# Optimization experiments

Measured on AMD Instinct MI355X. Metric: run time of the kernel, lower is better.

## Reference

```python
import jax, jax.numpy as jnp
import numpy as np

NUM_CELLS = 1_000_000
NUM_NETS = 1_500_000
NUM_PINS = 6_000_000
BOARD = 1000.0   # board_size
GAMMA = 4.0      # LSE smoothing parameter from __init__


def setup_inputs() -> dict:
    key = jax.random.key(0)
    k1, k2, k3, k4 = jax.random.split(key, 4)
    cells_pos = jax.random.uniform(k1, (NUM_CELLS, 2), dtype=jnp.float32) * BOARD
    pin_offsets = jax.random.normal(k2, (NUM_PINS, 2), dtype=jnp.float32) * 0.5
    pin_cell = jax.random.randint(k3, (NUM_PINS,), 0, NUM_CELLS)
    pin_net = jnp.sort(jax.random.randint(k4, (NUM_PINS,), 0, NUM_NETS))
    return {"cells_pos": cells_pos, "pin_offsets": pin_offsets,
            "pin_cell": pin_cell, "pin_net": pin_net}


def _seg_lse(vals, seg, num_segments, gamma):
    # per-segment  gamma * logsumexp(vals / gamma), numerically stable.
    m = jax.ops.segment_max(vals, seg, num_segments=num_segments,
                            indices_are_sorted=True)
    empty = jnp.isneginf(m)                     # segments with no pins
    m_safe = jnp.where(empty, 0.0, m)
    s = jax.ops.segment_sum(jnp.exp((vals - m_safe[seg]) / gamma), seg,
                            num_segments=num_segments, indices_are_sorted=True)
    lse = m_safe + gamma * jnp.log(jnp.maximum(s, 1e-30))
    return jnp.where(empty, 0.0, lse)


def reference(cells_pos, pin_offsets, pin_cell, pin_net):
    # pin coordinates: cell center + pin offset  (matches calculate_lse_wl)
    xs = cells_pos[pin_cell, 0] + pin_offsets[:, 0]   # [P]
    ys = cells_pos[pin_cell, 1] + pin_offsets[:, 1]   # [P]
    g = jnp.float32(GAMMA)
    total = (_seg_lse(xs, pin_net, NUM_NETS, g)
             + _seg_lse(-xs, pin_net, NUM_NETS, g)
             + _seg_lse(ys, pin_net, NUM_NETS, g)
             + _seg_lse(-ys, pin_net, NUM_NETS, g)).sum()
    return total
```

## Files before the change

kernel.cpp:

```cpp
#include <hip/hip_runtime.h>
#include <math.h>

#define NUM_NETS_C 1500000
#define GAMMA_C 4.0f

#define ENC_SCALE 65.535f
#define DEC_SCALE (1.0f / 65.535f)

__global__ void __launch_bounds__(256)
pack_cells(const float4* __restrict__ cells2,
           uint2* __restrict__ packed2,
           int C2) {
    int i = blockIdx.x * blockDim.x + threadIdx.x;
    if (i >= C2) return;
    float4 cp = cells2[i];
    unsigned ux0 = (unsigned)__float2int_rn(cp.x * ENC_SCALE);
    unsigned uy0 = (unsigned)__float2int_rn(cp.y * ENC_SCALE);
    unsigned ux1 = (unsigned)__float2int_rn(cp.z * ENC_SCALE);
    unsigned uy1 = (unsigned)__float2int_rn(cp.w * ENC_SCALE);
    packed2[i] = make_uint2((uy0 << 16) | ux0, (uy1 << 16) | ux1);
}

__global__ void __launch_bounds__(256)
build_starts(const int* __restrict__ pin_net,
             int* __restrict__ net_start,
             int P, int N) {
    int t = blockIdx.x * blockDim.x + threadIdx.x;
    int base = t * 4;
    if (base > P) return;
    if (base == P) {
        int prev = pin_net[P - 1];
        for (int n = prev + 1; n <= N; ++n) net_start[n] = P;
        return;
    }
    int4 c4 = *reinterpret_cast<const int4*>(pin_net + base);
    int prev = (base == 0) ? -1 : pin_net[base - 1];
    int c[4] = {c4.x, c4.y, c4.z, c4.w};
    #pragma unroll
    for (int k = 0; k < 4; ++k) {
        int cu = c[k];
        for (int n = prev + 1; n <= cu; ++n) net_start[n] = base + k;
        prev = cu;
    }
}

__device__ __forceinline__ void upd(float& m, float& s, float v, float inv_g) {
    float nm = fmaxf(m, v);
    s = s * __expf((m - nm) * inv_g) + __expf((v - nm) * inv_g);
    m = nm;
}

__global__ void __launch_bounds__(256)
net_lse(const unsigned int* __restrict__ packed,
        const float2* __restrict__ offs,
        const int* __restrict__ pin_cell,
        const int* __restrict__ net_start,
        float* __restrict__ out, int N) {
    const float g = GAMMA_C;
    const float inv_g = 1.0f / GAMMA_C;

    int n = blockIdx.x * blockDim.x + threadIdx.x;
    float wl = 0.0f;
    if (n < N) {
        int s0 = net_start[n];
        int e0 = net_start[n + 1];
        if (e0 > s0) {
            float mx  = -INFINITY, sx  = 0.0f;
            float mnx = -INFINITY, snx = 0.0f;
            float my  = -INFINITY, sy  = 0.0f;
            float mny = -INFINITY, sny = 0.0f;
            for (int i = s0; i < e0; ++i) {
                int c          = pin_cell[i];
                unsigned int p = packed[c];
                float2 od      = offs[i];
                float x = (float)(p & 0xFFFFu) * DEC_SCALE + od.x;
                float y = (float)(p >> 16)     * DEC_SCALE + od.y;
                upd(mx,  sx,  x,  inv_g);
                upd(mnx, snx, -x, inv_g);
                upd(my,  sy,  y,  inv_g);
                upd(mny, sny, -y, inv_g);
            }
            wl = (mx + mnx + my + mny)
               + g * (__logf(sx) + __logf(snx) + __logf(sy) + __logf(sny));
        }
    }

    #pragma unroll
    for (int o = 32; o > 0; o >>= 1) wl += __shfl_down(wl, o, 64);

    __shared__ float warp_sums[4];
    int lane = threadIdx.x & 63;
    int wid  = threadIdx.x >> 6;
    if (lane == 0) warp_sums[wid] = wl;
    __syncthreads();
    if (threadIdx.x == 0) {
        float bs = warp_sums[0] + warp_sums[1] + warp_sums[2] + warp_sums[3];
        atomicAdd(out, bs);
    }
}

extern "C" void kernel_launch(void* const* d_in, const int* in_sizes, int n_in,
                              void* d_out, int out_size, void* d_ws, size_t ws_size,
                              hipStream_t stream) {
    const float2* cells    = (const float2*)d_in[0];
    const float2* offs     = (const float2*)d_in[1];
    const int*    pin_cell = (const int*)d_in[2];
    const int*    pin_net  = (const int*)d_in[3];
    float*        out      = (float*)d_out;

    const int P = in_sizes[2];
    const int C = in_sizes[0] / 2;
    const int N = NUM_NETS_C;

    int* net_start = (int*)d_ws;
    size_t ns_bytes = ((size_t)(N + 1) * sizeof(int) + 255) & ~(size_t)255;
    unsigned int* packed = (unsigned int*)((char*)d_ws + ns_bytes);

    hipMemsetAsync(d_out, 0, sizeof(float), stream);

    {
        int C2 = C / 2;
        int block = 256, grid = (C2 + block - 1) / block;
        pack_cells<<<grid, block, 0, stream>>>((const float4*)cells,
                                               (uint2*)packed, C2);
    }
    {
        int threads = P / 4 + 1;
        int block = 256, grid = (threads + block - 1) / block;
        build_starts<<<grid, block, 0, stream>>>(pin_net, net_start, P, N);
    }
    {
        int block = 256, grid = (N + block - 1) / block;
        net_lse<<<grid, block, 0, stream>>>(packed, offs, pin_cell,
                                            net_start, out, N);
    }
}
```

Baseline: 228.1 us.

## Replace per-net loop with pin-parallel wavefront segmented scan and carry combine

Drops the net_start build pass and the thread-per-net serial loop. Each pin is handled by one lane, exp terms are computed without a max shift using double-precision exponent splitting, and per-net sums are formed with a wavefront segmented scan. Nets spanning wavefront boundaries are merged by a small combine kernel. This aims to remove load imbalance and the extra pass, but double shuffles and FP64 adds cost throughput and assume no overflow without max subtraction.

```diff
diff --git a/kernel.cpp b/kernel.cpp
--- a/kernel.cpp
+++ b/kernel.cpp
@@ -1,19 +1,19 @@
 #include <hip/hip_runtime.h>
 #include <math.h>
 
-#define NUM_NETS_C 1500000
-#define GAMMA_C 4.0f
-
+#define GAMMA_LN2 2.7725887222397811f
+#define INV4LN2   0.36067376022224085f
 #define ENC_SCALE 65.535f
 #define DEC_SCALE (1.0f / 65.535f)
 
+typedef float floatx4 __attribute__((ext_vector_type(4)));
+typedef float floatx2 __attribute__((ext_vector_type(2)));
+
 __global__ void __launch_bounds__(256)
-pack_cells(const float4* __restrict__ cells2,
-           uint2* __restrict__ packed2,
-           int C2) {
+pack_cells(const floatx4* __restrict__ cells2, uint2* __restrict__ packed2, int C2) {
     int i = blockIdx.x * blockDim.x + threadIdx.x;
     if (i >= C2) return;
-    float4 cp = cells2[i];
+    floatx4 cp = __builtin_nontemporal_load(cells2 + i);
     unsigned ux0 = (unsigned)__float2int_rn(cp.x * ENC_SCALE);
     unsigned uy0 = (unsigned)__float2int_rn(cp.y * ENC_SCALE);
     unsigned ux1 = (unsigned)__float2int_rn(cp.z * ENC_SCALE);
@@ -21,117 +21,156 @@
     packed2[i] = make_uint2((uy0 << 16) | ux0, (uy1 << 16) | ux1);
 }
 
-__global__ void __launch_bounds__(256)
-build_starts(const int* __restrict__ pin_net,
-             int* __restrict__ net_start,
-             int P, int N) {
-    int t = blockIdx.x * blockDim.x + threadIdx.x;
-    int base = t * 4;
-    if (base > P) return;
-    if (base == P) {
-        int prev = pin_net[P - 1];
-        for (int n = prev + 1; n <= N; ++n) net_start[n] = P;
-        return;
-    }
-    int4 c4 = *reinterpret_cast<const int4*>(pin_net + base);
-    int prev = (base == 0) ? -1 : pin_net[base - 1];
-    int c[4] = {c4.x, c4.y, c4.z, c4.w};
-    #pragma unroll
-    for (int k = 0; k < 4; ++k) {
-        int cu = c[k];
-        for (int n = prev + 1; n <= cu; ++n) net_start[n] = base + k;
-        prev = cu;
-    }
+__device__ __forceinline__ double eterm(float t) {
+    float kf = floorf(t);
+    float f  = t - kf;
+    float m  = exp2f(f);
+    long long bits = ((long long)(1023 + (int)kf)) << 52;
+    return (double)m * __longlong_as_double(bits);
 }
 
-__device__ __forceinline__ void upd(float& m, float& s, float v, float inv_g) {
-    float nm = fmaxf(m, v);
-    s = s * __expf((m - nm) * inv_g) + __expf((v - nm) * inv_g);
-    m = nm;
+__device__ __forceinline__ float lterm(double s) {
+    long long u = __double_as_longlong(s);
+    int e = (int)((u >> 52) & 0x7FF) - 1023;
+    long long mbits = (u & 0x000FFFFFFFFFFFFFll) | 0x3FF0000000000000ll;
+    float mf = (float)__longlong_as_double(mbits);
+    return (float)e + __log2f(mf);
 }
 
 __global__ void __launch_bounds__(256)
-net_lse(const unsigned int* __restrict__ packed,
-        const float2* __restrict__ offs,
-        const int* __restrict__ pin_cell,
-        const int* __restrict__ net_start,
-        float* __restrict__ out, int N) {
-    const float g = GAMMA_C;
-    const float inv_g = 1.0f / GAMMA_C;
+pin_pass(const unsigned* __restrict__ packed,
+         const floatx2*  __restrict__ offs,
+         const int*      __restrict__ pin_cell,
+         const int*      __restrict__ pin_net,
+         int*    __restrict__ ownNet,
+         double* __restrict__ ownS,
+         double* __restrict__ cfS,
+         int*    __restrict__ cfCont,
+         float*  __restrict__ out, int P, int W) {
+    int lane = threadIdx.x & 63;
+    int w    = blockIdx.x * 4 + (threadIdx.x >> 6);
+    float wl = 0.0f;
 
-    int n = blockIdx.x * blockDim.x + threadIdx.x;
-    float wl = 0.0f;
-    if (n < N) {
-        int s0 = net_start[n];
-        int e0 = net_start[n + 1];
-        if (e0 > s0) {
-            float mx  = -INFINITY, sx  = 0.0f;
-            float mnx = -INFINITY, snx = 0.0f;
-            float my  = -INFINITY, sy  = 0.0f;
-            float mny = -INFINITY, sny = 0.0f;
-            for (int i = s0; i < e0; ++i) {
-                int c          = pin_cell[i];
-                unsigned int p = packed[c];
-                float2 od      = offs[i];
-                float x = (float)(p & 0xFFFFu) * DEC_SCALE + od.x;
-                float y = (float)(p >> 16)     * DEC_SCALE + od.y;
-                upd(mx,  sx,  x,  inv_g);
-                upd(mnx, snx, -x, inv_g);
-                upd(my,  sy,  y,  inv_g);
-                upd(mny, sny, -y, inv_g);
+    if (w < W) {
+        int base = w * 64;
+        int p = base + lane;
+        int g = __builtin_nontemporal_load(pin_net + p);
+        int c = __builtin_nontemporal_load(pin_cell + p);
+        floatx2 of = __builtin_nontemporal_load(offs + p);
+        unsigned pk = packed[c];
+        float x = (float)(pk & 0xFFFFu) * DEC_SCALE + of.x;
+        float y = (float)(pk >> 16)     * DEC_SCALE + of.y;
+        float tx = x * INV4LN2, ty = y * INV4LN2;
+        double sx  = eterm(tx),  snx = eterm(-tx);
+        double sy  = eterm(ty),  sny = eterm(-ty);
+
+        int gup = __shfl_up(g, 1, 64);
+        int gdn = __shfl_down(g, 1, 64);
+        int c0 = 0;
+        if (lane == 0) c0 = (base > 0) && (pin_net[base - 1] == g);
+        c0 = __shfl(c0, 0, 64);
+        int c63 = 0;
+        if (lane == 63) c63 = (p + 1 < P) && (pin_net[p + 1] == g);
+        c63 = __shfl(c63, 63, 64);
+        bool head  = (lane == 0) || (g != gup);
+        bool isEnd = (lane == 63) || (g != gdn);
+        bool single = (__ballot(head) == 1ull);
+
+        int ss = head ? lane : 0;
+        #pragma unroll
+        for (int d = 1; d <= 32; d <<= 1) {
+            int t = __shfl_up(ss, d, 64);
+            if (lane >= d) ss = max(ss, t);
+        }
+        #pragma unroll
+        for (int d = 1; d <= 32; d <<= 1) {
+            double t0 = __shfl_up(sx,  d, 64);
+            double t1 = __shfl_up(snx, d, 64);
+            double t2 = __shfl_up(sy,  d, 64);
+            double t3 = __shfl_up(sny, d, 64);
+            if (lane - d >= ss) { sx += t0; snx += t1; sy += t2; sny += t3; }
+        }
+
+        if (isEnd) {
+            bool sOK = (ss > 0) || (!c0);
+            bool eOK = (lane < 63) || (!c63);
+            if (sOK && eOK)
+                wl = GAMMA_LN2 * (lterm(sx) + lterm(snx) + lterm(sy) + lterm(sny));
+            if (ss == 0) {
+                cfCont[w] = (single && c0 && c63) ? 1 : 0;
+                cfS[4*w+0] = sx; cfS[4*w+1] = snx; cfS[4*w+2] = sy; cfS[4*w+3] = sny;
             }
-            wl = (mx + mnx + my + mny)
-               + g * (__logf(sx) + __logf(snx) + __logf(sy) + __logf(sny));
+            if (lane == 63) {
+                bool owner = c63 && !(single && c0);
+                ownNet[w] = owner ? g : -1;
+                ownS[4*w+0] = sx; ownS[4*w+1] = snx; ownS[4*w+2] = sy; ownS[4*w+3] = sny;
+            }
         }
     }
 
     #pragma unroll
     for (int o = 32; o > 0; o >>= 1) wl += __shfl_down(wl, o, 64);
+    __shared__ float ws4[4];
+    if ((threadIdx.x & 63) == 0) ws4[threadIdx.x >> 6] = wl;
+    __syncthreads();
+    if (threadIdx.x == 0) atomicAdd(out, ws4[0] + ws4[1] + ws4[2] + ws4[3]);
+}
 
-    __shared__ float warp_sums[4];
-    int lane = threadIdx.x & 63;
-    int wid  = threadIdx.x >> 6;
-    if (lane == 0) warp_sums[wid] = wl;
+__global__ void __launch_bounds__(256)
+combine(const int* __restrict__ ownNet, const double* __restrict__ ownS,
+        const double* __restrict__ cfS, const int* __restrict__ cfCont,
+        float* __restrict__ out, int W) {
+    int w = blockIdx.x * blockDim.x + threadIdx.x;
+    float wl = 0.0f;
+    if (w < W && ownNet[w] >= 0) {
+        double S0 = ownS[4*w+0], S1 = ownS[4*w+1], S2 = ownS[4*w+2], S3 = ownS[4*w+3];
+        for (int v = w + 1; v < W; ++v) {
+            S0 += cfS[4*v+0]; S1 += cfS[4*v+1]; S2 += cfS[4*v+2]; S3 += cfS[4*v+3];
+            if (!cfCont[v]) break;
+        }
+        wl = GAMMA_LN2 * (lterm(S0) + lterm(S1) + lterm(S2) + lterm(S3));
+    }
+    #pragma unroll
+    for (int o = 32; o > 0; o >>= 1) wl += __shfl_down(wl, o, 64);
+    __shared__ float ws4[4];
+    if ((threadIdx.x & 63) == 0) ws4[threadIdx.x >> 6] = wl;
     __syncthreads();
-    if (threadIdx.x == 0) {
-        float bs = warp_sums[0] + warp_sums[1] + warp_sums[2] + warp_sums[3];
-        atomicAdd(out, bs);
-    }
+    if (threadIdx.x == 0) atomicAdd(out, ws4[0] + ws4[1] + ws4[2] + ws4[3]);
 }
 
 extern "C" void kernel_launch(void* const* d_in, const int* in_sizes, int n_in,
                               void* d_out, int out_size, void* d_ws, size_t ws_size,
                               hipStream_t stream) {
     const float2* cells    = (const float2*)d_in[0];
-    const float2* offs     = (const float2*)d_in[1];
+    const floatx2* offs    = (const floatx2*)d_in[1];
     const int*    pin_cell = (const int*)d_in[2];
     const int*    pin_net  = (const int*)d_in[3];
-    float*        out      = (float*)d_out;
 
     const int P = in_sizes[2];
     const int C = in_sizes[0] / 2;
-    const int N = NUM_NETS_C;
+    const int W = P / 64;
 
-    int* net_start = (int*)d_ws;
-    size_t ns_bytes = ((size_t)(N + 1) * sizeof(int) + 255) & ~(size_t)255;
-    unsigned int* packed = (unsigned int*)((char*)d_ws + ns_bytes);
+    char* base = (char*)d_ws;
+    size_t o = 0;
+    unsigned* packed = (unsigned*)(base + o); o += (size_t)C * 4;          o = (o + 255) & ~(size_t)255;
+    double*   ownS   = (double*)(base + o);   o += (size_t)W * 4 * 8;      o = (o + 255) & ~(size_t)255;
+    double*   cfS    = (double*)(base + o);   o += (size_t)W * 4 * 8;      o = (o + 255) & ~(size_t)255;
+    int*      ownNet = (int*)(base + o);      o += (size_t)W * 4;          o = (o + 255) & ~(size_t)255;
+    int*      cfCont = (int*)(base + o);
 
-    hipMemsetAsync(d_out, 0, sizeof(float), stream);
+    (void)hipMemsetAsync(d_out, 0, sizeof(float), stream);
 
-    {
-        int C2 = C / 2;
-        int block = 256, grid = (C2 + block - 1) / block;
-        pack_cells<<<grid, block, 0, stream>>>((const float4*)cells,
-                                               (uint2*)packed, C2);
+    {   int C2 = C / 2;
+        pack_cells<<<(C2 + 255) / 256, 256, 0, stream>>>((const floatx4*)cells,
+                                                         (uint2*)packed, C2);
     }
-    {
-        int threads = P / 4 + 1;
-        int block = 256, grid = (threads + block - 1) / block;
-        build_starts<<<grid, block, 0, stream>>>(pin_net, net_start, P, N);
+    {   int grid = (W + 3) / 4;
+        pin_pass<<<grid, 256, 0, stream>>>(packed, offs, pin_cell, pin_net,
+                                           ownNet, ownS, cfS, cfCont,
+                                           (float*)d_out, P, W);
     }
-    {
-        int block = 256, grid = (N + block - 1) / block;
-        net_lse<<<grid, block, 0, stream>>>(packed, offs, pin_cell,
-                                            net_start, out, N);
+    {   int grid = (W + 255) / 256;
+        combine<<<grid, 256, 0, stream>>>(ownNet, ownS, cfS, cfCont,
+                                          (float*)d_out, W);
     }
 }
```

After: 424.8 us. +86.2%, slower.
